# Performance work log

Measured on AMD Instinct MI355X. Metric: run time of the kernel, lower is better.

Reference implementation:

```python
import jax, jax.numpy as jnp
import numpy as np

B, C, K, F = 16, 64, 128, 6
HORIZON_S = 3.0  # conflict_horizon_s default
EPS = 1e-06


def setup_inputs() -> dict:
    rng = np.random.default_rng(0)
    # base adjacency: sparse random directed graph, zero diagonal
    A = (rng.random((B, K, K)) < 0.05).astype(np.float32)
    A[:, np.arange(K), np.arange(K)] = 0.0
    # candidates: exactly one unordered-pair edit (state in {0:none,1:i->j,2:j->i})
    cand = np.repeat(A[:, None], C, axis=1).copy()
    i = rng.integers(0, K - 1, (B, C))
    j = i + 1 + (rng.integers(0, K - 1, (B, C)) % (K - 1 - i))
    state = rng.integers(0, 3, (B, C))
    bidx = np.arange(B)[:, None] * np.ones((1, C), dtype=np.int64)
    cidx = np.ones((B, 1), dtype=np.int64) * np.arange(C)[None, :]
    cand[bidx, cidx, i, j] = (state == 1).astype(np.float32)
    cand[bidx, cidx, j, i] = (state == 2).astype(np.float32)
    cand[:, 0] = A  # candidate 0 is NOOP (keep A_t)
    # agent features: (x, y, yaw, vx, vy, pad)
    feat = rng.normal(size=(B, K, F)).astype(np.float32)
    feat[..., 0:2] *= 20.0  # spread positions over ~40m
    mask = (rng.random((B, K)) > 0.1).astype(np.float32)
    return {
        "A_t": jnp.asarray(A),
        "candidate_A": jnp.asarray(cand),
        "agent_feat": jnp.asarray(feat),
        "agent_mask": jnp.asarray(mask),
    }


def _edit_tokens(A_t, candidate_A):
    # vectorized version of EBSTM.extract_edit_tokens
    Bn, Cn, Kn, _ = candidate_A.shape
    base = A_t > 0.5                      # [B,K,K]
    cb = candidate_A > 0.5                # [B,C,K,K]
    diff = cb != base[:, None]            # [B,C,K,K]
    upper = jnp.triu(jnp.ones((Kn, Kn), dtype=bool), k=1)
    pairdiff = (diff | jnp.swapaxes(diff, -1, -2)) & upper
    flat = pairdiff.reshape(Bn, Cn, Kn * Kn)
    changed = flat.any(-1)                # [B,C]
    idx = jnp.argmax(flat, axis=-1)       # first changed pair in row-major (i,j) order
    i = idx // Kn
    j = idx % Kn
    barange = jnp.arange(Bn)[:, None]
    carange = jnp.arange(Cn)[None, :]
    b_ij = base[barange, i, j]
    b_ji = base[barange, j, i]
    c_ij = cb[barange, carange, i, j]
    c_ji = cb[barange, carange, j, i]
    prev = jnp.where(b_ij & ~b_ji, 1, jnp.where(b_ji & ~b_ij, 2, 0))
    nxt = jnp.where(c_ij & ~c_ji, 1, jnp.where(c_ji & ~c_ij, 2, 0))
    tokens = jnp.stack([i, j, prev, nxt], axis=-1).astype(jnp.int32)
    return tokens * changed[..., None].astype(jnp.int32)


def _relation_state3(cb):
    # cb: bool [B,C,K,K]
    at = jnp.swapaxes(cb, -1, -2)
    return ((cb & ~at).astype(jnp.int32) * 1
            + (~cb & at).astype(jnp.int32) * 2
            + (cb & at).astype(jnp.int32) * 3)


def _batched_acyclic(cb, agent_mask):
    # vectorized Kahn zero-indegree peel, matching EBSTM._is_acyclic semantics:
    #  - indegree counts edges from ALL sources (valid or not)
    #  - only valid nodes are ever removed
    #  - special case: <=1 valid node is acyclic
    Bn, Cn, Kn, _ = cb.shape
    valid = (agent_mask > 0.5)[:, None, :]           # [B,1,K]
    Ai = cb.astype(jnp.int32)                        # [B,C,K,K]
    indeg = Ai.sum(axis=-2) * valid.astype(jnp.int32)  # [B,C,K]
    removed = jnp.zeros((Bn, Cn, Kn), dtype=bool)

    def body(t, carry):
        indeg, removed = carry
        rem = valid & (~removed) & (indeg == 0)
        dec = jnp.einsum('bci,bcij->bcj', rem.astype(jnp.int32), Ai)
        return indeg - dec, removed | rem

    indeg, removed = jax.lax.fori_loop(0, Kn, body, (indeg, removed))
    vcount = valid.astype(jnp.int32).sum(-1)          # [B,1]
    return (removed.astype(jnp.int32).sum(-1) == vcount) | (vcount <= 1)


def _pair_dists(agent_feat):
    pos = agent_feat[..., 0:2]
    vel = agent_feat[..., 3:5]
    # _pair_distance: d[b,i,j] = |pos_i - pos_j|
    d = jnp.linalg.norm(pos[:, :, None] - pos[:, None, :], axis=-1)
    # _pair_closest_approach_distance: r[b,i,j] = pos_j - pos_i
    r = pos[:, None, :] - pos[:, :, None]
    v = vel[:, None, :] - vel[:, :, None]
    vv = (v * v).sum(-1)
    rv = (r * v).sum(-1)
    t_star = jnp.clip(-rv / (vv + EPS), 0.0, HORIZON_S)
    dmin = jnp.linalg.norm(r + v * t_star[..., None], axis=-1)
    eye = jnp.eye(dmin.shape[-1], dtype=bool)[None]
    dmin = jnp.where(eye, jnp.inf, dmin)
    return jnp.stack([d, dmin], axis=0)  # [2,B,K,K]


def reference(A_t, candidate_A, agent_feat, agent_mask):
    cb = candidate_A > 0.5
    tokens = _edit_tokens(A_t, candidate_A)          # [B,C,4] int32
    rel = _relation_state3(cb)                       # [B,C,K,K] int32
    acyclic = _batched_acyclic(cb, agent_mask)       # [B,C] bool
    dists = _pair_dists(agent_feat)                  # [2,B,K,K] float32
    return tokens, rel, acyclic, dists
```

## Files before the change

kernel.cpp:

```cpp
#include <hip/hip_runtime.h>
#include <cstdint>
#include <math.h>

#define KN 128
#define BATCH 16
#define CAND 64

typedef float vfloat4 __attribute__((ext_vector_type(4)));

static constexpr size_t TOK_OFF = 0;
static constexpr size_t REL_OFF = (size_t)BATCH * CAND * 4;
static constexpr size_t ACY_OFF = REL_OFF + (size_t)BATCH * CAND * KN * KN;
static constexpr size_t DST_OFF = ACY_OFF + (size_t)BATCH * CAND;

#define DIAG_BIG 1.0e30f

__global__ __launch_bounds__(256) void prep_kernel(const float* __restrict__ A_t,
                                                   const float* __restrict__ feat,
                                                   uint32_t* __restrict__ bits,
                                                   float* __restrict__ out) {
    int t = threadIdx.x;
    {
        int tid  = blockIdx.x * 256 + t;
        int wave = tid >> 6;
        int lane = tid & 63;
        int half = wave & 1;
        int row  = wave >> 1;
        float v = A_t[(size_t)row * KN + half * 64 + lane];
        unsigned long long m = __ballot(v > 0.5f);
        if (lane == 0) {
            bits[row * 4 + half * 2]     = (uint32_t)m;
            bits[row * 4 + half * 2 + 1] = (uint32_t)(m >> 32);
        }
    }
    {
        int bi = 2 * blockIdx.x + (t >> 7);
        int b2 = bi >> 7, i = bi & 127, j = t & 127;
        const float* fi = feat + (size_t)bi * 6;
        const float* fj = feat + (size_t)(b2 * KN + j) * 6;
        float pix = fi[0], piy = fi[1], vix = fi[3], viy = fi[4];
        float pjx = fj[0], pjy = fj[1], vjx = fj[3], vjy = fj[4];
        float dx = pix - pjx, dy = piy - pjy;
        float d = sqrtf(dx * dx + dy * dy);
        float rx = pjx - pix, ry = pjy - piy;
        float vx = vjx - vix, vy = vjy - viy;
        float vv = vx * vx + vy * vy;
        float rv = rx * vx + ry * vy;
        float ts = fminf(fmaxf(-rv / (vv + 1e-6f), 0.0f), 3.0f);
        float mx = rx + vx * ts, my = ry + vy * ts;
        float dmin = (i == j) ? DIAG_BIG : sqrtf(mx * mx + my * my);
        float* o = out + DST_OFF;
        __builtin_nontemporal_store(d,    o + (size_t)(b2 * KN + i) * KN + j);
        __builtin_nontemporal_store(dmin, o + (size_t)((BATCH + b2) * KN + i) * KN + j);
    }
}

__global__ __launch_bounds__(256) void main_kernel(const float* __restrict__ cand,
                                                   const float* __restrict__ mask,
                                                   const uint32_t* __restrict__ baseBits,
                                                   float* __restrict__ out) {
    __shared__ uint32_t adj[KN][5];
    __shared__ uint32_t adjT[KN][6];
    __shared__ uint32_t baseB[KN][4];
    __shared__ uint32_t validW[4];
    __shared__ uint32_t remW[4];
    __shared__ uint32_t removedW[4];
    __shared__ int      minIdx;

    const int t    = threadIdx.x;
    const int lane = t & 63;
    const int wave = t >> 6;
    const int bc   = blockIdx.x;
    const int b    = bc >> 6;

    const float* cptr = cand + (size_t)bc * (KN * KN);
    float* relp = out + REL_OFF + (size_t)bc * (KN * KN);

    float4 c[16];
    const int sub = lane & 31;
    #pragma unroll
    for (int m = 0; m < 16; ++m) {
        int r = (m * 4 + wave) * 2 + (lane >> 5);
        c[m] = ((const float4*)(cptr + (size_t)r * KN))[sub];
    }

    if (t == 0) minIdx = 0x7fffffff;
    if (t < 4)  removedW[t] = 0;

    for (int w = t; w < 512; w += 256) {
        baseB[w >> 2][w & 3] = baseBits[b * 512 + w];
    }

    if (wave < 2) {
        float mv = mask[b * KN + wave * 64 + lane];
        unsigned long long m = __ballot(mv > 0.5f);
        if (lane == 0) {
            validW[wave * 2]     = (uint32_t)m;
            validW[wave * 2 + 1] = (uint32_t)(m >> 32);
        }
    }

    #pragma unroll
    for (int m = 0; m < 16; ++m) {
        int r = (m * 4 + wave) * 2 + (lane >> 5);
        const float4 v = c[m];
        uint32_t nib = (v.x > 0.5f ? 1u : 0u) | (v.y > 0.5f ? 2u : 0u) |
                       (v.z > 0.5f ? 4u : 0u) | (v.w > 0.5f ? 8u : 0u);
        uint32_t word = nib << (4 * (sub & 7));
        word |= __shfl_xor(word, 1);
        word |= __shfl_xor(word, 2);
        word |= __shfl_xor(word, 4);
        if ((lane & 7) == 0) adj[r][sub >> 3] = word;
    }
    __syncthreads();

    {
        const int h = wave >> 1, q = wave & 1;
        uint32_t rw0 = adj[h * 64 + lane][q * 2];
        uint32_t rw1 = adj[h * 64 + lane][q * 2 + 1];
        uint32_t myLo = 0, myHi = 0;
        #pragma unroll
        for (int cc = 0; cc < 64; ++cc) {
            uint32_t w = (cc < 32) ? rw0 : rw1;
            unsigned long long m = __ballot((w >> (cc & 31)) & 1u);
            if (lane == cc) { myLo = (uint32_t)m; myHi = (uint32_t)(m >> 32); }
        }
        adjT[q * 64 + lane][2 * h]     = myLo;
        adjT[q * 64 + lane][2 * h + 1] = myHi;
    }
    __syncthreads();

    uint32_t cT0 = 0, cT1 = 0, cT2 = 0, cT3 = 0;
    int  indeg = 0;
    bool validT = false;
    if (t < KN) {
        cT0 = adjT[t][0]; cT1 = adjT[t][1]; cT2 = adjT[t][2]; cT3 = adjT[t][3];
        validT = (validW[t >> 5] >> (t & 31)) & 1u;
        indeg = validT ? (__popc(cT0) + __popc(cT1) + __popc(cT2) + __popc(cT3)) : 0;
    }

    auto rel_expand = [&]() {
        #pragma unroll
        for (int m = 0; m < 16; ++m) {
            int q  = t + 256 * m;
            int i  = q >> 5;
            int j0 = (q & 31) * 4;
            int iw = j0 >> 5, sh = j0 & 31;
            uint32_t wij = adj[i][iw];
            uint32_t wti = adjT[i][iw];
            vfloat4 o;
            o.x = (float)(((wij >> (sh + 0)) & 1u) + 2u * ((wti >> (sh + 0)) & 1u));
            o.y = (float)(((wij >> (sh + 1)) & 1u) + 2u * ((wti >> (sh + 1)) & 1u));
            o.z = (float)(((wij >> (sh + 2)) & 1u) + 2u * ((wti >> (sh + 2)) & 1u));
            o.w = (float)(((wij >> (sh + 3)) & 1u) + 2u * ((wti >> (sh + 3)) & 1u));
            __builtin_nontemporal_store(o, ((vfloat4*)relp) + q);
        }
    };

    auto logic_phase = [&]() {
        for (int idx = t; idx < 512; idx += 256) {
            int i = idx >> 2, k = idx & 3;
            uint32_t diff = adj[i][k] ^ baseB[i][k];
            if (diff) {
                int base = k * 32;
                uint32_t up, low;
                if (i < base)            { up = diff; low = 0u; }
                else if (i >= base + 31) { up = 0u; low = (i > base + 31) ? diff : (diff & 0x7fffffffu); }
                else {
                    int s = i - base;
                    up  = diff & (0xffffffffu << (s + 1));
                    low = diff & ((1u << s) - 1u);
                }
                int c1 = 0x7fffffff, c2 = 0x7fffffff;
                if (up)  c1 = (i << 7) | (base + __builtin_ctz(up));
                if (low) { int cc2 = base + __builtin_ctz(low); c2 = (cc2 << 7) | i; }
                int cm = min(c1, c2);
                if (cm != 0x7fffffff) atomicMin(&minIdx, cm);
            }
        }
        __syncthreads();

        if (t == 0) {
            float* tok = out + TOK_OFF + (size_t)bc * 4;
            int mi = minIdx;
            if (mi != 0x7fffffff) {
                int i = mi >> 7, j = mi & 127;
                uint32_t b_ij = (baseB[i][j >> 5] >> (j & 31)) & 1u;
                uint32_t b_ji = (baseB[j][i >> 5] >> (i & 31)) & 1u;
                uint32_t c_ij = (adj[i][j >> 5] >> (j & 31)) & 1u;
                uint32_t c_ji = (adj[j][i >> 5] >> (i & 31)) & 1u;
                int prev = (b_ij && !b_ji) ? 1 : ((b_ji && !b_ij) ? 2 : 0);
                int nxt  = (c_ij && !c_ji) ? 1 : ((c_ji && !c_ij) ? 2 : 0);
                tok[0] = (float)i; tok[1] = (float)j; tok[2] = (float)prev; tok[3] = (float)nxt;
            } else {
                tok[0] = 0.f; tok[1] = 0.f; tok[2] = 0.f; tok[3] = 0.f;
            }
        }

        bool removed = false;
        for (int it = 0; it < KN; ++it) {
            bool rem = (t < KN) && validT && !removed && (indeg == 0);
            unsigned long long m = __ballot(rem);
            if (wave < 2 && lane == 0) {
                remW[wave * 2]     = (uint32_t)m;
                remW[wave * 2 + 1] = (uint32_t)(m >> 32);
            }
            __syncthreads();
            uint32_t r0 = remW[0], r1 = remW[1], r2 = remW[2], r3 = remW[3];
            if ((r0 | r1 | r2 | r3) == 0u) break;
            if (t < 4) removedW[t] |= remW[t];
            if (t < KN) {
                indeg -= __popc(r0 & cT0) + __popc(r1 & cT1) +
                         __popc(r2 & cT2) + __popc(r3 & cT3);
                removed = removed || rem;
            }
            __syncthreads();
        }
        __syncthreads();

        if (t == 0) {
            int rc = __popc(removedW[0]) + __popc(removedW[1]) + __popc(removedW[2]) + __popc(removedW[3]);
            int vc = __popc(validW[0]) + __popc(validW[1]) + __popc(validW[2]) + __popc(validW[3]);
            out[ACY_OFF + bc] = ((rc == vc) || (vc <= 1)) ? 1.0f : 0.0f;
        }
    };

    if ((bc & 1) == 0) {
        rel_expand();
        logic_phase();
    } else {
        logic_phase();
        rel_expand();
    }
}

extern "C" void kernel_launch(void* const* d_in, const int* in_sizes, int n_in,
                              void* d_out, int out_size, void* d_ws, size_t ws_size,
                              hipStream_t stream) {
    const float* A_t  = (const float*)d_in[0];
    const float* cand = (const float*)d_in[1];
    const float* feat = (const float*)d_in[2];
    const float* mask = (const float*)d_in[3];
    float* out = (float*)d_out;
    uint32_t* bits = (uint32_t*)d_ws;

    prep_kernel<<<1024, 256, 0, stream>>>(A_t, feat, bits, out);
    main_kernel<<<BATCH * CAND, 256, 0, stream>>>(cand, mask, bits, out);
}
```

Before: 121.0 us.

## Run edit-token and acyclicity logic in one wave; dynamic chunked rel stores

Moves the diff-scan, token extraction and Kahn's topological-sort loop into wave 0 alone, using ballots and shuffles instead of block-wide __syncthreads and shared atomics. Each lane handles two nodes, so no block barriers are needed per iteration. Meanwhile the other three waves, plus wave 0 once it finishes, grab 256-element chunks of the rel expansion through a shared atomic counter. This is meant to hide the serial logic behind the bulk rel output stores, at the cost of a single wave doing all the logic.

Result: slower. 126.0 us (+4.1%).

```diff
diff --git a/kernel.cpp b/kernel.cpp
--- a/kernel.cpp
+++ b/kernel.cpp
@@ -62,10 +62,7 @@
     __shared__ uint32_t adj[KN][5];
     __shared__ uint32_t adjT[KN][6];
     __shared__ uint32_t baseB[KN][4];
-    __shared__ uint32_t validW[4];
-    __shared__ uint32_t remW[4];
-    __shared__ uint32_t removedW[4];
-    __shared__ int      minIdx;
+    __shared__ int storeChunk;
 
     const int t    = threadIdx.x;
     const int lane = t & 63;
@@ -84,19 +81,13 @@
         c[m] = ((const float4*)(cptr + (size_t)r * KN))[sub];
     }
 
-    if (t == 0) minIdx = 0x7fffffff;
-    if (t < 4)  removedW[t] = 0;
-
-    for (int w = t; w < 512; w += 256) {
-        baseB[w >> 2][w & 3] = baseBits[b * 512 + w];
-    }
-
-    if (wave < 2) {
-        float mv = mask[b * KN + wave * 64 + lane];
-        unsigned long long m = __ballot(mv > 0.5f);
-        if (lane == 0) {
-            validW[wave * 2]     = (uint32_t)m;
-            validW[wave * 2 + 1] = (uint32_t)(m >> 32);
+    if (t == 0) storeChunk = 0;
+
+    if (wave == 0) {
+        #pragma unroll
+        for (int s = 0; s < 8; ++s) {
+            int w = lane + 64 * s;
+            baseB[w >> 2][w & 3] = baseBits[b * 512 + w];
         }
     }
 
@@ -130,19 +121,90 @@
     }
     __syncthreads();
 
-    uint32_t cT0 = 0, cT1 = 0, cT2 = 0, cT3 = 0;
-    int  indeg = 0;
-    bool validT = false;
-    if (t < KN) {
-        cT0 = adjT[t][0]; cT1 = adjT[t][1]; cT2 = adjT[t][2]; cT3 = adjT[t][3];
-        validT = (validW[t >> 5] >> (t & 31)) & 1u;
-        indeg = validT ? (__popc(cT0) + __popc(cT1) + __popc(cT2) + __popc(cT3)) : 0;
-    }
-
-    auto rel_expand = [&]() {
-        #pragma unroll
-        for (int m = 0; m < 16; ++m) {
-            int q  = t + 256 * m;
+    if (wave == 0) {
+        unsigned long long v1 = __ballot(mask[b * KN + lane]      > 0.5f);
+        unsigned long long v2 = __ballot(mask[b * KN + 64 + lane] > 0.5f);
+
+        int cmin = 0x7fffffff;
+        #pragma unroll
+        for (int s = 0; s < 8; ++s) {
+            int idx = lane + 64 * s;
+            int i = idx >> 2, k = idx & 3;
+            uint32_t diff = adj[i][k] ^ baseB[i][k];
+            if (diff) {
+                int base = k * 32;
+                uint32_t up, low;
+                if (i < base)            { up = diff; low = 0u; }
+                else if (i >= base + 31) { up = 0u; low = (i > base + 31) ? diff : (diff & 0x7fffffffu); }
+                else {
+                    int sft = i - base;
+                    up  = diff & (0xffffffffu << (sft + 1));
+                    low = diff & ((1u << sft) - 1u);
+                }
+                int c1 = 0x7fffffff, c2 = 0x7fffffff;
+                if (up)  c1 = (i << 7) | (base + __builtin_ctz(up));
+                if (low) { int cc2 = base + __builtin_ctz(low); c2 = (cc2 << 7) | i; }
+                cmin = min(cmin, min(c1, c2));
+            }
+        }
+        #pragma unroll
+        for (int off = 32; off > 0; off >>= 1) cmin = min(cmin, __shfl_down(cmin, off));
+
+        if (lane == 0) {
+            float* tok = out + TOK_OFF + (size_t)bc * 4;
+            if (cmin != 0x7fffffff) {
+                int i = cmin >> 7, j = cmin & 127;
+                uint32_t b_ij = (baseB[i][j >> 5] >> (j & 31)) & 1u;
+                uint32_t b_ji = (baseB[j][i >> 5] >> (i & 31)) & 1u;
+                uint32_t c_ij = (adj[i][j >> 5] >> (j & 31)) & 1u;
+                uint32_t c_ji = (adj[j][i >> 5] >> (i & 31)) & 1u;
+                int prev = (b_ij && !b_ji) ? 1 : ((b_ji && !b_ij) ? 2 : 0);
+                int nxt  = (c_ij && !c_ji) ? 1 : ((c_ji && !c_ij) ? 2 : 0);
+                tok[0] = (float)i; tok[1] = (float)j; tok[2] = (float)prev; tok[3] = (float)nxt;
+            } else {
+                tok[0] = 0.f; tok[1] = 0.f; tok[2] = 0.f; tok[3] = 0.f;
+            }
+        }
+
+        uint32_t a0 = adjT[lane][0],      a1 = adjT[lane][1];
+        uint32_t a2 = adjT[lane][2],      a3 = adjT[lane][3];
+        uint32_t d0 = adjT[lane + 64][0], d1 = adjT[lane + 64][1];
+        uint32_t d2 = adjT[lane + 64][2], d3 = adjT[lane + 64][3];
+        const bool val1 = (v1 >> lane) & 1ull;
+        const bool val2 = (v2 >> lane) & 1ull;
+        int id1 = val1 ? (__popc(a0) + __popc(a1) + __popc(a2) + __popc(a3)) : 0;
+        int id2 = val2 ? (__popc(d0) + __popc(d1) + __popc(d2) + __popc(d3)) : 0;
+        bool rm1 = false, rm2 = false;
+        for (int it = 0; it < KN; ++it) {
+            bool r1 = val1 && !rm1 && (id1 == 0);
+            bool r2 = val2 && !rm2 && (id2 == 0);
+            unsigned long long m1 = __ballot(r1);
+            unsigned long long m2 = __ballot(r2);
+            if ((m1 | m2) == 0ull) break;
+            rm1 = rm1 || r1;
+            rm2 = rm2 || r2;
+            uint32_t r0w = (uint32_t)m1, r1w = (uint32_t)(m1 >> 32);
+            uint32_t r2w = (uint32_t)m2, r3w = (uint32_t)(m2 >> 32);
+            id1 -= __popc(r0w & a0) + __popc(r1w & a1) + __popc(r2w & a2) + __popc(r3w & a3);
+            id2 -= __popc(r0w & d0) + __popc(r1w & d1) + __popc(r2w & d2) + __popc(r3w & d3);
+        }
+        unsigned long long rmm1 = __ballot(rm1);
+        unsigned long long rmm2 = __ballot(rm2);
+        if (lane == 0) {
+            int rc = __popcll(rmm1) + __popcll(rmm2);
+            int vc = __popcll(v1) + __popcll(v2);
+            out[ACY_OFF + bc] = ((rc == vc) || (vc <= 1)) ? 1.0f : 0.0f;
+        }
+    }
+
+    for (;;) {
+        int ch = 0;
+        if (lane == 0) ch = atomicAdd(&storeChunk, 1);
+        ch = __shfl(ch, 0);
+        if (ch >= 16) break;
+        #pragma unroll
+        for (int ii = 0; ii < 4; ++ii) {
+            int q  = ch * 256 + ii * 64 + lane;
             int i  = q >> 5;
             int j0 = (q & 31) * 4;
             int iw = j0 >> 5, sh = j0 & 31;
@@ -155,82 +217,6 @@
             o.w = (float)(((wij >> (sh + 3)) & 1u) + 2u * ((wti >> (sh + 3)) & 1u));
             __builtin_nontemporal_store(o, ((vfloat4*)relp) + q);
         }
-    };
-
-    auto logic_phase = [&]() {
-        for (int idx = t; idx < 512; idx += 256) {
-            int i = idx >> 2, k = idx & 3;
-            uint32_t diff = adj[i][k] ^ baseB[i][k];
-            if (diff) {
-                int base = k * 32;
-                uint32_t up, low;
-                if (i < base)            { up = diff; low = 0u; }
-                else if (i >= base + 31) { up = 0u; low = (i > base + 31) ? diff : (diff & 0x7fffffffu); }
-                else {
-                    int s = i - base;
-                    up  = diff & (0xffffffffu << (s + 1));
-                    low = diff & ((1u << s) - 1u);
-                }
-                int c1 = 0x7fffffff, c2 = 0x7fffffff;
-                if (up)  c1 = (i << 7) | (base + __builtin_ctz(up));
-                if (low) { int cc2 = base + __builtin_ctz(low); c2 = (cc2 << 7) | i; }
-                int cm = min(c1, c2);
-                if (cm != 0x7fffffff) atomicMin(&minIdx, cm);
-            }
-        }
-        __syncthreads();
-
-        if (t == 0) {
-            float* tok = out + TOK_OFF + (size_t)bc * 4;
-            int mi = minIdx;
-            if (mi != 0x7fffffff) {
-                int i = mi >> 7, j = mi & 127;
-                uint32_t b_ij = (baseB[i][j >> 5] >> (j & 31)) & 1u;
-                uint32_t b_ji = (baseB[j][i >> 5] >> (i & 31)) & 1u;
-                uint32_t c_ij = (adj[i][j >> 5] >> (j & 31)) & 1u;
-                uint32_t c_ji = (adj[j][i >> 5] >> (i & 31)) & 1u;
-                int prev = (b_ij && !b_ji) ? 1 : ((b_ji && !b_ij) ? 2 : 0);
-                int nxt  = (c_ij && !c_ji) ? 1 : ((c_ji && !c_ij) ? 2 : 0);
-                tok[0] = (float)i; tok[1] = (float)j; tok[2] = (float)prev; tok[3] = (float)nxt;
-            } else {
-                tok[0] = 0.f; tok[1] = 0.f; tok[2] = 0.f; tok[3] = 0.f;
-            }
-        }
-
-        bool removed = false;
-        for (int it = 0; it < KN; ++it) {
-            bool rem = (t < KN) && validT && !removed && (indeg == 0);
-            unsigned long long m = __ballot(rem);
-            if (wave < 2 && lane == 0) {
-                remW[wave * 2]     = (uint32_t)m;
-                remW[wave * 2 + 1] = (uint32_t)(m >> 32);
-            }
-            __syncthreads();
-            uint32_t r0 = remW[0], r1 = remW[1], r2 = remW[2], r3 = remW[3];
-            if ((r0 | r1 | r2 | r3) == 0u) break;
-            if (t < 4) removedW[t] |= remW[t];
-            if (t < KN) {
-                indeg -= __popc(r0 & cT0) + __popc(r1 & cT1) +
-                         __popc(r2 & cT2) + __popc(r3 & cT3);
-                removed = removed || rem;
-            }
-            __syncthreads();
-        }
-        __syncthreads();
-
-        if (t == 0) {
-            int rc = __popc(removedW[0]) + __popc(removedW[1]) + __popc(removedW[2]) + __popc(removedW[3]);
-            int vc = __popc(validW[0]) + __popc(validW[1]) + __popc(validW[2]) + __popc(validW[3]);
-            out[ACY_OFF + bc] = ((rc == vc) || (vc <= 1)) ? 1.0f : 0.0f;
-        }
-    };
-
-    if ((bc & 1) == 0) {
-        rel_expand();
-        logic_phase();
-    } else {
-        logic_phase();
-        rel_expand();
     }
 }
 
```
